# Kernel tuning notes

Hardware: AMD Instinct MI355X
Metric: run time of the kernel (lower is better)

The kernel has to match this reference:

```python
import jax, jax.numpy as jnp
import numpy as np

N = 50000      # nodes
E = 800000     # edges
G = 64         # graphs in batch
H = 256        # hidden_channels
CE = 128       # coord embed dim = H//2
OTH = 6        # in_channels - 3
ED = 8         # edge_dim
EE = 128       # edge_embedding_dim
GD = 16        # global_dim
L = 3          # num_layers


def setup_inputs() -> dict:
    key = jax.random.key(0)
    ks = jax.random.split(key, 24)
    s = 0.05
    inp = {
        "x": jax.random.normal(ks[0], (N, 9), jnp.float32),
        "edge_index": jax.random.randint(ks[1], (2, E), 0, N),
        "batch": jnp.sort(jax.random.randint(ks[2], (N,), 0, G)),
        "edge_attr": jax.random.normal(ks[3], (E, ED), jnp.float32),
        "global_x": jax.random.normal(ks[4], (G, GD), jnp.float32),
        # coordinate embedder (Linear 3->128 + relu)
        "coord_W": jax.random.normal(ks[5], (3, CE), jnp.float32) * s,
        "coord_b": jnp.zeros((CE,), jnp.float32),
        # node_mlp (Linear 6->128 + relu)
        "node_W": jax.random.normal(ks[6], (OTH, CE), jnp.float32) * s,
        "node_b": jnp.zeros((CE,), jnp.float32),
        # edge processor (Linear 8->128 + relu) and projection 128->256
        "edge_W": jax.random.normal(ks[7], (ED, EE), jnp.float32) * s,
        "edge_b": jnp.zeros((EE,), jnp.float32),
        "proj_W": jax.random.normal(ks[8], (EE, H), jnp.float32) * s,
        "proj_b": jnp.zeros((H,), jnp.float32),
        # stacked GCN layer weights
        "gcn_W": jax.random.normal(ks[9], (L, H, H), jnp.float32) * s,
        "gcn_b": jnp.zeros((L, H), jnp.float32),
        # attention pooling
        "attn_w": jax.random.normal(ks[10], (H,), jnp.float32) * s,
        "attn_b": jnp.zeros((), jnp.float32),
        # global_mlp: Linear 16->256, relu, Linear 256->256
        "gmlp_W1": jax.random.normal(ks[11], (GD, H), jnp.float32) * s,
        "gmlp_b1": jnp.zeros((H,), jnp.float32),
        "gmlp_W2": jax.random.normal(ks[12], (H, H), jnp.float32) * s,
        "gmlp_b2": jnp.zeros((H,), jnp.float32),
        # fc_out: Linear 512->256, relu, Linear 256->1
        "fc_W1": jax.random.normal(ks[13], (2 * H, H), jnp.float32) * s,
        "fc_b1": jnp.zeros((H,), jnp.float32),
        "fc_W2": jax.random.normal(ks[14], (H, 1), jnp.float32) * s,
        "fc_b2": jnp.zeros((1,), jnp.float32),
    }
    return inp


def _segsum(v, idx, num):
    return jax.ops.segment_sum(v, idx, num_segments=num)


def reference(x, edge_index, batch, edge_attr, global_x,
              coord_W, coord_b, node_W, node_b, edge_W, edge_b,
              proj_W, proj_b, gcn_W, gcn_b, attn_w, attn_b,
              gmlp_W1, gmlp_b1, gmlp_W2, gmlp_b2,
              fc_W1, fc_b1, fc_W2, fc_b2):
    relu = jax.nn.relu
    # --- node embedding: coords + other features ---
    coord_emb = relu(x[:, :3] @ coord_W + coord_b)          # [N, 128]
    other_emb = relu(x[:, 3:] @ node_W + node_b)            # [N, 128]
    x_emb = jnp.concatenate([coord_emb, other_emb], axis=1)  # [N, 256]

    # --- edge embedding, aggregated to target nodes (index_add over col) ---
    edge_emb = relu(edge_attr @ edge_W + edge_b) @ proj_W + proj_b  # [E, 256]
    col0 = edge_index[1]
    node_msg = _segsum(edge_emb, col0, N)                    # [N, 256]

    # --- GCN normalization with self-loops ---
    sl = jnp.arange(N)
    row = jnp.concatenate([edge_index[0], sl])
    col = jnp.concatenate([edge_index[1], sl])
    deg = _segsum(jnp.ones_like(col, jnp.float32), col, N)   # >= 1
    dnorm = jax.lax.rsqrt(deg)
    efac = (dnorm[row] * dnorm[col])[:, None]                # [E+N, 1]

    # --- stacked GCN layers (edge messages re-added each layer, per source) ---
    for i in range(L):
        x_in = x_emb + node_msg
        h = x_in @ gcn_W[i]                                  # [N, 256]
        x_emb = _segsum(h[row] * efac, col, N) + gcn_b[i]
        if i < L - 1:
            x_emb = relu(x_emb)

    # --- attention pooling (per-graph softmax over batch index) ---
    scores = x_emb @ attn_w + attn_b                         # [N]
    m = jax.ops.segment_max(scores, batch, num_segments=G)
    e = jnp.exp(scores - m[batch])
    denom = _segsum(e, batch, G)
    attn = e / denom[batch]
    graph_emb = _segsum(x_emb * attn[:, None], batch, G)     # [G, 256]

    # --- global features + head ---
    g = relu(global_x @ gmlp_W1 + gmlp_b1) @ gmlp_W2 + gmlp_b2
    hcat = jnp.concatenate([graph_emb, g], axis=-1)          # [G, 512]
    out = relu(hcat @ fc_W1 + fc_b1) @ fc_W2 + fc_b2         # [G, 1]
    return out
```

## Files before the change

### kernel.cpp

```cpp
#include <hip/hip_runtime.h>


typedef float f32x4 __attribute__((ext_vector_type(4)));
typedef short s16x8 __attribute__((ext_vector_type(8)));

__device__ __forceinline__ unsigned short f2bf(float f) {
  union { float f; unsigned u; } v{f};
  unsigned r = v.u + 0x7fff + ((v.u >> 16) & 1);
  return (unsigned short)(r >> 16);
}
__device__ __forceinline__ float bf2f(unsigned short s) {
  union { unsigned u; float f; } v{(unsigned)s << 16};
  return v.f;
}
__device__ __forceinline__ float blo(unsigned u) {
  union { unsigned x; float f; } v{u << 16};
  return v.f;
}
__device__ __forceinline__ float bhi(unsigned u) {
  union { unsigned x; float f; } v{u & 0xffff0000u};
  return v.f;
}
__device__ __forceinline__ unsigned pk2(float a, float b) {
  return (unsigned)f2bf(a) | ((unsigned)f2bf(b) << 16);
}

__global__ void node_embed_kernel(const float* __restrict__ x,
                                  const float* __restrict__ coord_W, const float* __restrict__ coord_b,
                                  const float* __restrict__ node_W, const float* __restrict__ node_b,
                                  short* __restrict__ x0, int N) {
  int tid = threadIdx.x;
  int node = blockIdx.x * 8 + (tid >> 5);
  if (node >= N) return;
  int ch0 = (tid & 31) * 8;
  const float* xr = x + (size_t)node * 9;
  float a[8];
  if (ch0 < 128) {
    float4 b0 = *(const float4*)&coord_b[ch0];
    float4 b1 = *(const float4*)&coord_b[ch0 + 4];
    a[0]=b0.x; a[1]=b0.y; a[2]=b0.z; a[3]=b0.w; a[4]=b1.x; a[5]=b1.y; a[6]=b1.z; a[7]=b1.w;
#pragma unroll
    for (int k = 0; k < 3; k++) {
      float xv = xr[k];
      float4 w0 = *(const float4*)&coord_W[k * 128 + ch0];
      float4 w1 = *(const float4*)&coord_W[k * 128 + ch0 + 4];
      a[0] = fmaf(xv, w0.x, a[0]); a[1] = fmaf(xv, w0.y, a[1]);
      a[2] = fmaf(xv, w0.z, a[2]); a[3] = fmaf(xv, w0.w, a[3]);
      a[4] = fmaf(xv, w1.x, a[4]); a[5] = fmaf(xv, w1.y, a[5]);
      a[6] = fmaf(xv, w1.z, a[6]); a[7] = fmaf(xv, w1.w, a[7]);
    }
  } else {
    int c0 = ch0 - 128;
    float4 b0 = *(const float4*)&node_b[c0];
    float4 b1 = *(const float4*)&node_b[c0 + 4];
    a[0]=b0.x; a[1]=b0.y; a[2]=b0.z; a[3]=b0.w; a[4]=b1.x; a[5]=b1.y; a[6]=b1.z; a[7]=b1.w;
#pragma unroll
    for (int k = 0; k < 6; k++) {
      float xv = xr[3 + k];
      float4 w0 = *(const float4*)&node_W[k * 128 + c0];
      float4 w1 = *(const float4*)&node_W[k * 128 + c0 + 4];
      a[0] = fmaf(xv, w0.x, a[0]); a[1] = fmaf(xv, w0.y, a[1]);
      a[2] = fmaf(xv, w0.z, a[2]); a[3] = fmaf(xv, w0.w, a[3]);
      a[4] = fmaf(xv, w1.x, a[4]); a[5] = fmaf(xv, w1.y, a[5]);
      a[6] = fmaf(xv, w1.z, a[6]); a[7] = fmaf(xv, w1.w, a[7]);
    }
  }
  uint4 o;
  o.x = pk2(fmaxf(a[0], 0.f), fmaxf(a[1], 0.f));
  o.y = pk2(fmaxf(a[2], 0.f), fmaxf(a[3], 0.f));
  o.z = pk2(fmaxf(a[4], 0.f), fmaxf(a[5], 0.f));
  o.w = pk2(fmaxf(a[6], 0.f), fmaxf(a[7], 0.f));
  *(uint4*)&x0[(size_t)node * 256 + ch0] = o;
}

__global__ void count_kernel(const int* __restrict__ col, int* __restrict__ cnt, int E) {
  int e = blockIdx.x * 256 + threadIdx.x;
  if (e < E) atomicAdd(&cnt[col[e]], 1);
}

__global__ void breduce_kernel(const int* __restrict__ cnt, int* __restrict__ partials, int N) {
  __shared__ int red[256];
  int t = threadIdx.x;
  int i = blockIdx.x * 256 + t;
  int v = (i < N) ? cnt[i] : 0;
  red[t] = v;
  __syncthreads();
  for (int off = 128; off; off >>= 1) {
    if (t < off) red[t] += red[t + off];
    __syncthreads();
  }
  if (t == 0) partials[blockIdx.x] = red[0];
}

__global__ void scan_partials_kernel(int* __restrict__ partials, int nb) {
  __shared__ int s[1024];
  int t = threadIdx.x;
  for (int i = t; i < nb; i += 256) s[i] = partials[i];
  __syncthreads();
  if (t == 0) {
    int run = 0;
    for (int i = 0; i < nb; i++) { int c = s[i]; s[i] = run; run += c; }
  }
  __syncthreads();
  for (int i = t; i < nb; i += 256) partials[i] = s[i];
}

__global__ void scan_apply_kernel(const int* __restrict__ cnt, const int* __restrict__ partials,
                                  int* __restrict__ rowstart, float* __restrict__ dnorm,
                                  int* __restrict__ cursor, int N) {
  __shared__ int red[256];
  int t = threadIdx.x;
  int i = blockIdx.x * 256 + t;
  int v = (i < N) ? cnt[i] : 0;
  red[t] = v;
  __syncthreads();
  for (int off = 1; off < 256; off <<= 1) {
    int x = (t >= off) ? red[t - off] : 0;
    __syncthreads();
    red[t] += x;
    __syncthreads();
  }
  if (i < N) {
    int ex = red[t] - v + partials[blockIdx.x];
    rowstart[i] = ex;
    dnorm[i] = rsqrtf((float)(v + 1));
    cursor[i] = 0;
    if (i == N - 1) rowstart[N] = ex + v;
  }
}

__global__ void scatter_kernel(const int* __restrict__ row, const int* __restrict__ col,
                               const int* __restrict__ rowstart, int* __restrict__ cursor,
                               const float* __restrict__ dnorm,
                               int2* __restrict__ pk8, int* __restrict__ eids, int E) {
  int e = blockIdx.x * 256 + threadIdx.x;
  if (e >= E) return;
  int c = col[e], r = row[e];
  int p = atomicAdd(&cursor[c], 1);
  int slot = rowstart[c] + p;
  pk8[slot] = make_int2(r, __float_as_int(dnorm[r] * dnorm[c]));
  eids[slot] = e;
}

__global__ void wt_kernel(const float* __restrict__ gcn_W, const float* __restrict__ proj_W,
                          short* __restrict__ gcnWt, short* __restrict__ projWt) {
  int idx = blockIdx.x * 256 + threadIdx.x;
  if (idx < 3 * 65536) {
    int l = idx >> 16, r = idx & 65535, n = r >> 8, k = r & 255;
    gcnWt[idx] = (short)f2bf(gcn_W[l * 65536 + k * 256 + n]);
  } else {
    int j = idx - 3 * 65536;
    int n = j >> 7, k = j & 127;
    projWt[j] = (short)f2bf(proj_W[k * 256 + n]);
  }
}

__global__ void __launch_bounds__(256) edge_msg_kernel(
    const float* __restrict__ edge_attr, const int* __restrict__ eids,
    const int* __restrict__ rowstart,
    const float* __restrict__ edge_W, const float* __restrict__ edge_b,
    unsigned* __restrict__ msg128u, int N) {
  int lane = threadIdx.x & 63;
  int node = blockIdx.x * 4 + (threadIdx.x >> 6);
  if (node >= N) return;
  int ch0 = lane * 2;
  float wa[8], wb[8];
#pragma unroll
  for (int k = 0; k < 8; k++) {
    float2 w = *(const float2*)&edge_W[k * 128 + ch0];
    wa[k] = w.x; wb[k] = w.y;
  }
  float2 bb = *(const float2*)&edge_b[ch0];
  float acc0 = 0.f, acc1 = 0.f;
  int s = rowstart[node], s1 = rowstart[node + 1];
  const float4* ea4 = (const float4*)edge_attr;
  for (; s + 4 <= s1; s += 4) {
    int e0 = eids[s], e1 = eids[s + 1], e2 = eids[s + 2], e3 = eids[s + 3];
    float4 a00 = ea4[(size_t)e0 * 2], a01 = ea4[(size_t)e0 * 2 + 1];
    float4 a10 = ea4[(size_t)e1 * 2], a11 = ea4[(size_t)e1 * 2 + 1];
    float4 a20 = ea4[(size_t)e2 * 2], a21 = ea4[(size_t)e2 * 2 + 1];
    float4 a30 = ea4[(size_t)e3 * 2], a31 = ea4[(size_t)e3 * 2 + 1];
    float t0, t1;
#define EMLP(lo, hi)                                                        \
    t0 = bb.x; t1 = bb.y;                                                   \
    t0 = fmaf(lo.x, wa[0], t0); t1 = fmaf(lo.x, wb[0], t1);                 \
    t0 = fmaf(lo.y, wa[1], t0); t1 = fmaf(lo.y, wb[1], t1);                 \
    t0 = fmaf(lo.z, wa[2], t0); t1 = fmaf(lo.z, wb[2], t1);                 \
    t0 = fmaf(lo.w, wa[3], t0); t1 = fmaf(lo.w, wb[3], t1);                 \
    t0 = fmaf(hi.x, wa[4], t0); t1 = fmaf(hi.x, wb[4], t1);                 \
    t0 = fmaf(hi.y, wa[5], t0); t1 = fmaf(hi.y, wb[5], t1);                 \
    t0 = fmaf(hi.z, wa[6], t0); t1 = fmaf(hi.z, wb[6], t1);                 \
    t0 = fmaf(hi.w, wa[7], t0); t1 = fmaf(hi.w, wb[7], t1);                 \
    acc0 += fmaxf(t0, 0.f); acc1 += fmaxf(t1, 0.f);
    EMLP(a00, a01)
    EMLP(a10, a11)
    EMLP(a20, a21)
    EMLP(a30, a31)
  }
  for (; s < s1; s++) {
    int e = eids[s];
    float4 lo = ea4[(size_t)e * 2], hi = ea4[(size_t)e * 2 + 1];
    float t0, t1;
    EMLP(lo, hi)
  }
#undef EMLP
  msg128u[(size_t)node * 64 + lane] = pk2(acc0, acc1);
}

__global__ void __launch_bounds__(256) proj_gemm_mfma(
    const short* __restrict__ msg128, const short* __restrict__ projWt,
    const float* __restrict__ proj_b, const int* __restrict__ cnt,
    short* __restrict__ node_msg, int N) {
  __shared__ short As[64][136];
  __shared__ short Bs[64][136];
  int tid = threadIdx.x;
  int n0 = blockIdx.x * 64;
  int cb = blockIdx.y * 64;
  for (int i = tid; i < 64 * 32; i += 256) {
    int r = i >> 5, c4 = (i & 31) << 2;
    int n = n0 + r;
    uint2 v = make_uint2(0, 0);
    if (n < N) v = *(const uint2*)&msg128[(size_t)n * 128 + c4];
    *(uint2*)&As[r][c4] = v;
    *(uint2*)&Bs[r][c4] = *(const uint2*)&projWt[(size_t)(cb + r) * 128 + c4];
  }
  __syncthreads();
  int wave = tid >> 6, lane = tid & 63;
  int mrow = wave * 16 + (lane & 15);
  int brow = lane & 15;
  int kgrp = (lane >> 4) * 8;
  f32x4 acc[4];
#pragma unroll
  for (int i = 0; i < 4; i++) acc[i] = (f32x4){0.f, 0.f, 0.f, 0.f};
#pragma unroll
  for (int kk = 0; kk < 4; kk++) {
    s16x8 a = *(const s16x8*)&As[mrow][kk * 32 + kgrp];
#pragma unroll
    for (int nf = 0; nf < 4; nf++) {
      s16x8 b = *(const s16x8*)&Bs[nf * 16 + brow][kk * 32 + kgrp];
      acc[nf] = __builtin_amdgcn_mfma_f32_16x16x32_bf16(a, b, acc[nf], 0, 0, 0);
    }
  }
  int orow0 = wave * 16 + (lane >> 4) * 4;
  int ocol = lane & 15;
#pragma unroll
  for (int r = 0; r < 4; r++) {
    int n = n0 + orow0 + r;
    if (n < N) {
      float cn = (float)cnt[n];
#pragma unroll
      for (int nf = 0; nf < 4; nf++) {
        int c = cb + nf * 16 + ocol;
        node_msg[(size_t)n * 256 + c] = (short)f2bf(acc[nf][r] + cn * proj_b[c]);
      }
    }
  }
}

__global__ void __launch_bounds__(256) gcn_gemm_add_mfma(
    const short* __restrict__ X, const short* __restrict__ M,
    const short* __restrict__ Wt, short* __restrict__ Hout, int N) {
  __shared__ short As[64][264];
  __shared__ short Bs[64][264];
  int tid = threadIdx.x;
  int n0 = blockIdx.x * 64;
  int cb = blockIdx.y * 64;
  for (int i = tid; i < 64 * 64; i += 256) {
    int r = i >> 6, c4 = (i & 63) << 2;
    int n = n0 + r;
    uint2 o = make_uint2(0, 0);
    if (n < N) {
      uint2 xv = *(const uint2*)&X[(size_t)n * 256 + c4];
      uint2 mv = *(const uint2*)&M[(size_t)n * 256 + c4];
      o.x = pk2(blo(xv.x) + blo(mv.x), bhi(xv.x) + bhi(mv.x));
      o.y = pk2(blo(xv.y) + blo(mv.y), bhi(xv.y) + bhi(mv.y));
    }
    *(uint2*)&As[r][c4] = o;
    *(uint2*)&Bs[r][c4] = *(const uint2*)&Wt[(size_t)(cb + r) * 256 + c4];
  }
  __syncthreads();
  int wave = tid >> 6, lane = tid & 63;
  int mrow = wave * 16 + (lane & 15);
  int brow = lane & 15;
  int kgrp = (lane >> 4) * 8;
  f32x4 acc[4];
#pragma unroll
  for (int i = 0; i < 4; i++) acc[i] = (f32x4){0.f, 0.f, 0.f, 0.f};
#pragma unroll
  for (int kk = 0; kk < 8; kk++) {
    s16x8 a = *(const s16x8*)&As[mrow][kk * 32 + kgrp];
#pragma unroll
    for (int nf = 0; nf < 4; nf++) {
      s16x8 b = *(const s16x8*)&Bs[nf * 16 + brow][kk * 32 + kgrp];
      acc[nf] = __builtin_amdgcn_mfma_f32_16x16x32_bf16(a, b, acc[nf], 0, 0, 0);
    }
  }
  int orow0 = wave * 16 + (lane >> 4) * 4;
  int ocol = lane & 15;
#pragma unroll
  for (int nf = 0; nf < 4; nf++) {
#pragma unroll
    for (int r = 0; r < 4; r++) {
      int n = n0 + orow0 + r;
      if (n < N) Hout[(size_t)n * 256 + cb + nf * 16 + ocol] = (short)f2bf(acc[nf][r]);
    }
  }
}

__global__ void __launch_bounds__(256) gcn_gemm_mfma(
    const short* __restrict__ Xin, const short* __restrict__ Wt,
    short* __restrict__ Hout, int N) {
  __shared__ short As[64][264];
  __shared__ short Bs[64][264];
  int tid = threadIdx.x;
  int n0 = blockIdx.x * 64;
  int cb = blockIdx.y * 64;
  for (int i = tid; i < 64 * 64; i += 256) {
    int r = i >> 6, c4 = (i & 63) << 2;
    int n = n0 + r;
    uint2 v = make_uint2(0, 0);
    if (n < N) v = *(const uint2*)&Xin[(size_t)n * 256 + c4];
    *(uint2*)&As[r][c4] = v;
    *(uint2*)&Bs[r][c4] = *(const uint2*)&Wt[(size_t)(cb + r) * 256 + c4];
  }
  __syncthreads();
  int wave = tid >> 6, lane = tid & 63;
  int mrow = wave * 16 + (lane & 15);
  int brow = lane & 15;
  int kgrp = (lane >> 4) * 8;
  f32x4 acc[4];
#pragma unroll
  for (int i = 0; i < 4; i++) acc[i] = (f32x4){0.f, 0.f, 0.f, 0.f};
#pragma unroll
  for (int kk = 0; kk < 8; kk++) {
    s16x8 a = *(const s16x8*)&As[mrow][kk * 32 + kgrp];
#pragma unroll
    for (int nf = 0; nf < 4; nf++) {
      s16x8 b = *(const s16x8*)&Bs[nf * 16 + brow][kk * 32 + kgrp];
      acc[nf] = __builtin_amdgcn_mfma_f32_16x16x32_bf16(a, b, acc[nf], 0, 0, 0);
    }
  }
  int orow0 = wave * 16 + (lane >> 4) * 4;
  int ocol = lane & 15;
#pragma unroll
  for (int nf = 0; nf < 4; nf++) {
#pragma unroll
    for (int r = 0; r < 4; r++) {
      int n = n0 + orow0 + r;
      if (n < N) Hout[(size_t)n * 256 + cb + nf * 16 + ocol] = (short)f2bf(acc[nf][r]);
    }
  }
}

__global__ void __launch_bounds__(256) gcn_agg_kernel(
    const short* __restrict__ h, const int2* __restrict__ pk8,
    const int* __restrict__ rowstart, const float* __restrict__ dnorm,
    const float* __restrict__ b, const short* __restrict__ node_msg,
    short* __restrict__ xin, int N) {
  int lane = threadIdx.x & 63;
  int node = blockIdx.x * 4 + (threadIdx.x >> 6);
  if (node >= N) return;
  int ch0 = lane << 2;
  size_t rowb = (size_t)node * 256 + ch0;
  float dn = dnorm[node];
  float wgt = dn * dn;
  uint2 hv = *(const uint2*)&h[rowb];
  float a0 = blo(hv.x) * wgt, a1 = bhi(hv.x) * wgt;
  float a2 = blo(hv.y) * wgt, a3 = bhi(hv.y) * wgt;
  int s = rowstart[node], s1 = rowstart[node + 1];
  for (; s + 4 <= s1; s += 4) {
    int2 p0 = pk8[s], p1 = pk8[s + 1], p2 = pk8[s + 2], p3 = pk8[s + 3];
    float f0 = __int_as_float(p0.y), f1 = __int_as_float(p1.y);
    float f2 = __int_as_float(p2.y), f3 = __int_as_float(p3.y);
    uint2 v0 = *(const uint2*)&h[(size_t)p0.x * 256 + ch0];
    uint2 v1 = *(const uint2*)&h[(size_t)p1.x * 256 + ch0];
    uint2 v2 = *(const uint2*)&h[(size_t)p2.x * 256 + ch0];
    uint2 v3 = *(const uint2*)&h[(size_t)p3.x * 256 + ch0];
    a0 = fmaf(blo(v0.x), f0, a0); a1 = fmaf(bhi(v0.x), f0, a1);
    a2 = fmaf(blo(v0.y), f0, a2); a3 = fmaf(bhi(v0.y), f0, a3);
    a0 = fmaf(blo(v1.x), f1, a0); a1 = fmaf(bhi(v1.x), f1, a1);
    a2 = fmaf(blo(v1.y), f1, a2); a3 = fmaf(bhi(v1.y), f1, a3);
    a0 = fmaf(blo(v2.x), f2, a0); a1 = fmaf(bhi(v2.x), f2, a1);
    a2 = fmaf(blo(v2.y), f2, a2); a3 = fmaf(bhi(v2.y), f2, a3);
    a0 = fmaf(blo(v3.x), f3, a0); a1 = fmaf(bhi(v3.x), f3, a1);
    a2 = fmaf(blo(v3.y), f3, a2); a3 = fmaf(bhi(v3.y), f3, a3);
  }
  for (; s < s1; s++) {
    int2 p = pk8[s];
    float f = __int_as_float(p.y);
    uint2 v = *(const uint2*)&h[(size_t)p.x * 256 + ch0];
    a0 = fmaf(blo(v.x), f, a0); a1 = fmaf(bhi(v.x), f, a1);
    a2 = fmaf(blo(v.y), f, a2); a3 = fmaf(bhi(v.y), f, a3);
  }
  float4 bv = *(const float4*)&b[ch0];
  uint2 mv = *(const uint2*)&node_msg[rowb];
  float y0 = fmaxf(a0 + bv.x, 0.f) + blo(mv.x);
  float y1 = fmaxf(a1 + bv.y, 0.f) + bhi(mv.x);
  float y2 = fmaxf(a2 + bv.z, 0.f) + blo(mv.y);
  float y3 = fmaxf(a3 + bv.w, 0.f) + bhi(mv.y);
  uint2 o;
  o.x = pk2(y0, y1);
  o.y = pk2(y2, y3);
  *(uint2*)&xin[rowb] = o;
}

__global__ void __launch_bounds__(256) final_agg_kernel(
    const short* __restrict__ h, const int2* __restrict__ pk8,
    const int* __restrict__ rowstart, const float* __restrict__ dnorm,
    const float* __restrict__ b, short* __restrict__ x_emb,
    const float* __restrict__ attn_w, const float* __restrict__ attn_b,
    float* __restrict__ scores, int N) {
  int lane = threadIdx.x & 63;
  int node = blockIdx.x * 4 + (threadIdx.x >> 6);
  if (node >= N) return;
  int ch0 = lane << 2;
  size_t rowb = (size_t)node * 256 + ch0;
  float dn = dnorm[node];
  float wgt = dn * dn;
  uint2 hv = *(const uint2*)&h[rowb];
  float a0 = blo(hv.x) * wgt, a1 = bhi(hv.x) * wgt;
  float a2 = blo(hv.y) * wgt, a3 = bhi(hv.y) * wgt;
  int s = rowstart[node], s1 = rowstart[node + 1];
  for (; s + 4 <= s1; s += 4) {
    int2 p0 = pk8[s], p1 = pk8[s + 1], p2 = pk8[s + 2], p3 = pk8[s + 3];
    float f0 = __int_as_float(p0.y), f1 = __int_as_float(p1.y);
    float f2 = __int_as_float(p2.y), f3 = __int_as_float(p3.y);
    uint2 v0 = *(const uint2*)&h[(size_t)p0.x * 256 + ch0];
    uint2 v1 = *(const uint2*)&h[(size_t)p1.x * 256 + ch0];
    uint2 v2 = *(const uint2*)&h[(size_t)p2.x * 256 + ch0];
    uint2 v3 = *(const uint2*)&h[(size_t)p3.x * 256 + ch0];
    a0 = fmaf(blo(v0.x), f0, a0); a1 = fmaf(bhi(v0.x), f0, a1);
    a2 = fmaf(blo(v0.y), f0, a2); a3 = fmaf(bhi(v0.y), f0, a3);
    a0 = fmaf(blo(v1.x), f1, a0); a1 = fmaf(bhi(v1.x), f1, a1);
    a2 = fmaf(blo(v1.y), f1, a2); a3 = fmaf(bhi(v1.y), f1, a3);
    a0 = fmaf(blo(v2.x), f2, a0); a1 = fmaf(bhi(v2.x), f2, a1);
    a2 = fmaf(blo(v2.y), f2, a2); a3 = fmaf(bhi(v2.y), f2, a3);
    a0 = fmaf(blo(v3.x), f3, a0); a1 = fmaf(bhi(v3.x), f3, a1);
    a2 = fmaf(blo(v3.y), f3, a2); a3 = fmaf(bhi(v3.y), f3, a3);
  }
  for (; s < s1; s++) {
    int2 p = pk8[s];
    float f = __int_as_float(p.y);
    uint2 v = *(const uint2*)&h[(size_t)p.x * 256 + ch0];
    a0 = fmaf(blo(v.x), f, a0); a1 = fmaf(bhi(v.x), f, a1);
    a2 = fmaf(blo(v.y), f, a2); a3 = fmaf(bhi(v.y), f, a3);
  }
  float4 bv = *(const float4*)&b[ch0];
  a0 += bv.x; a1 += bv.y; a2 += bv.z; a3 += bv.w;
  uint2 o;
  o.x = pk2(a0, a1);
  o.y = pk2(a2, a3);
  *(uint2*)&x_emb[rowb] = o;
  float4 aw = *(const float4*)&attn_w[ch0];
  float p = a0 * aw.x + a1 * aw.y + a2 * aw.z + a3 * aw.w;
#pragma unroll
  for (int off = 32; off; off >>= 1) p += __shfl_down(p, off);
  if (lane == 0) scores[node] = p + attn_b[0];
}

__global__ void gse_kernel(const int* __restrict__ batch, int* __restrict__ gs,
                           int* __restrict__ ge, int N) {
  int i = blockIdx.x * 256 + threadIdx.x;
  if (i >= N) return;
  int g = batch[i];
  if (i == 0) gs[g] = 0;
  else {
    int gp = batch[i - 1];
    if (gp != g) { gs[g] = i; ge[gp] = i - 1; }
  }
  if (i == N - 1) ge[g] = N - 1;
}

__global__ void softmax_kernel(const float* __restrict__ scores, const int* __restrict__ gs,
                               const int* __restrict__ ge, float* __restrict__ wnode) {
  int g = blockIdx.x;
  int tid = threadIdx.x;
  __shared__ float red[256];
  int s0 = gs[g], e1 = ge[g];
  if (s0 > e1) return;
  int s1 = e1 + 1;
  float m = -1e30f;
  for (int i = s0 + tid; i < s1; i += 256) m = fmaxf(m, scores[i]);
  red[tid] = m;
  __syncthreads();
  for (int off = 128; off; off >>= 1) {
    if (tid < off) red[tid] = fmaxf(red[tid], red[tid + off]);
    __syncthreads();
  }
  m = red[0];
  __syncthreads();
  float d = 0.f;
  for (int i = s0 + tid; i < s1; i += 256) d += expf(scores[i] - m);
  red[tid] = d;
  __syncthreads();
  for (int off = 128; off; off >>= 1) {
    if (tid < off) red[tid] += red[tid + off];
    __syncthreads();
  }
  float rd = 1.f / red[0];
  for (int i = s0 + tid; i < s1; i += 256) wnode[i] = expf(scores[i] - m) * rd;
}

__global__ void __launch_bounds__(256) pool_sum_kernel(
    const short* __restrict__ x_emb, const float* __restrict__ wnode,
    const int* __restrict__ batch, float* __restrict__ graph_emb, int N) {
  __shared__ int sb[256];
  __shared__ float sw[256];
  int ch = threadIdx.x;
  int i0 = blockIdx.x * 256;
  int lim = min(256, N - i0);
  if (ch < lim) { sb[ch] = batch[i0 + ch]; sw[ch] = wnode[i0 + ch]; }
  __syncthreads();
  int curg = sb[0];
  float acc = 0.f;
  for (int j = 0; j < lim; j++) {
    int g = sb[j];
    if (g != curg) {
      atomicAdd(&graph_emb[(size_t)curg * 256 + ch], acc);
      acc = 0.f;
      curg = g;
    }
    acc = fmaf(bf2f((unsigned short)x_emb[(size_t)(i0 + j) * 256 + ch]), sw[j], acc);
  }
  atomicAdd(&graph_emb[(size_t)curg * 256 + ch], acc);
}

__global__ void head_kernel(const float* __restrict__ global_x, const float* __restrict__ graph_emb,
                            const float* __restrict__ W1, const float* __restrict__ b1,
                            const float* __restrict__ W2, const float* __restrict__ b2,
                            const float* __restrict__ fW1, const float* __restrict__ fb1,
                            const float* __restrict__ fW2, const float* __restrict__ fb2,
                            float* __restrict__ out) {
  int g = blockIdx.x;
  int ch = threadIdx.x;
  __shared__ float t1[256], g2s[256], t3s[256];
  float a = b1[ch];
  const float* gx = global_x + g * 16;
#pragma unroll
  for (int k = 0; k < 16; k++) a = fmaf(gx[k], W1[k * 256 + ch], a);
  t1[ch] = fmaxf(a, 0.f);
  __syncthreads();
  float bb = b2[ch];
  for (int k = 0; k < 256; k++) bb = fmaf(t1[k], W2[k * 256 + ch], bb);
  g2s[ch] = bb;
  __syncthreads();
  float c = fb1[ch];
  const float* ger = graph_emb + (size_t)g * 256;
  for (int k = 0; k < 256; k++) c = fmaf(ger[k], fW1[k * 256 + ch], c);
  for (int k = 0; k < 256; k++) c = fmaf(g2s[k], fW1[(256 + k) * 256 + ch], c);
  t3s[ch] = fmaxf(c, 0.f);
  __syncthreads();
  t1[ch] = t3s[ch] * fW2[ch];
  __syncthreads();
  for (int off = 128; off; off >>= 1) {
    if (ch < off) t1[ch] += t1[ch + off];
    __syncthreads();
  }
  if (ch == 0) out[g] = t1[0] + fb2[0];
}

extern "C" void kernel_launch(void* const* d_in, const int* in_sizes, int n_in,
                              void* d_out, int out_size, void* d_ws, size_t ws_size,
                              hipStream_t stream) {
  const float* x        = (const float*)d_in[0];
  const int*   ei       = (const int*)d_in[1];
  const int*   batch    = (const int*)d_in[2];
  const float* edge_attr= (const float*)d_in[3];
  const float* global_x = (const float*)d_in[4];
  const float* coord_W  = (const float*)d_in[5];
  const float* coord_b  = (const float*)d_in[6];
  const float* node_W   = (const float*)d_in[7];
  const float* node_b   = (const float*)d_in[8];
  const float* edge_W   = (const float*)d_in[9];
  const float* edge_b   = (const float*)d_in[10];
  const float* proj_W   = (const float*)d_in[11];
  const float* proj_b   = (const float*)d_in[12];
  const float* gcn_W    = (const float*)d_in[13];
  const float* gcn_b    = (const float*)d_in[14];
  const float* attn_w   = (const float*)d_in[15];
  const float* attn_b   = (const float*)d_in[16];
  const float* gmlp_W1  = (const float*)d_in[17];
  const float* gmlp_b1  = (const float*)d_in[18];
  const float* gmlp_W2  = (const float*)d_in[19];
  const float* gmlp_b2  = (const float*)d_in[20];
  const float* fc_W1    = (const float*)d_in[21];
  const float* fc_b1    = (const float*)d_in[22];
  const float* fc_W2    = (const float*)d_in[23];
  const float* fc_b2    = (const float*)d_in[24];

  const int N = in_sizes[0] / 9;
  const int E = in_sizes[3] / 8;
  const int G = in_sizes[4] / 16;
  const int NB = (N + 255) / 256;
  const int NM = (N + 63) / 64;

  char* w = (char*)d_ws;
  auto alloc = [&](size_t bytes) -> char* {
    char* p = w;
    w += (bytes + 255) & ~(size_t)255;
    return p;
  };
  short* x0       = (short*)alloc((size_t)N * 256 * 2);
  short* node_msg = (short*)alloc((size_t)N * 256 * 2);
  short* hA       = (short*)alloc((size_t)N * 256 * 2);
  short* hB       = (short*)alloc((size_t)N * 256 * 2);
  short* xinBuf   = (short*)alloc((size_t)N * 256 * 2);
  short* x_emb    = (short*)alloc((size_t)N * 256 * 2);
  short* msg128   = x_emb;
  int2*  pk8      = (int2*)alloc((size_t)E * 8);
  int*   eids     = (int*)alloc((size_t)E * 4);
  short* gcnWt    = (short*)alloc((size_t)3 * 65536 * 2);
  short* projWt   = (short*)alloc((size_t)256 * 128 * 2);
  int*   cnt      = (int*)alloc((size_t)N * 4);
  int*   rowstart = (int*)alloc((size_t)(N + 1) * 4);
  int*   cursor   = (int*)alloc((size_t)N * 4);
  float* dnorm    = (float*)alloc((size_t)N * 4);
  float* scores   = (float*)alloc((size_t)N * 4);
  float* wnode    = (float*)alloc((size_t)N * 4);
  int*   partials = (int*)alloc((size_t)NB * 4);
  int*   gs       = (int*)alloc((size_t)G * 4);
  int*   ge       = (int*)alloc((size_t)G * 4);
  float* graph_emb= (float*)alloc((size_t)G * 256 * 4);

  hipMemsetAsync(cnt, 0, (size_t)N * 4, stream);
  hipMemsetAsync(gs, 0x7f, (size_t)G * 4, stream);
  hipMemsetAsync(ge, 0xff, (size_t)G * 4, stream);
  hipMemsetAsync(graph_emb, 0, (size_t)G * 256 * 4, stream);

  wt_kernel<<<(3 * 65536 + 256 * 128 + 255) / 256, 256, 0, stream>>>(gcn_W, proj_W, gcnWt, projWt);
  node_embed_kernel<<<(N + 7) / 8, 256, 0, stream>>>(
      x, coord_W, coord_b, node_W, node_b, x0, N);
  count_kernel<<<(E + 255) / 256, 256, 0, stream>>>(ei + E, cnt, E);
  breduce_kernel<<<NB, 256, 0, stream>>>(cnt, partials, N);
  scan_partials_kernel<<<1, 256, 0, stream>>>(partials, NB);
  scan_apply_kernel<<<NB, 256, 0, stream>>>(cnt, partials, rowstart, dnorm, cursor, N);
  scatter_kernel<<<(E + 255) / 256, 256, 0, stream>>>(
      ei, ei + E, rowstart, cursor, dnorm, pk8, eids, E);
  edge_msg_kernel<<<(N + 3) / 4, 256, 0, stream>>>(
      edge_attr, eids, rowstart, edge_W, edge_b, (unsigned*)msg128, N);
  proj_gemm_mfma<<<dim3(NM, 4), 256, 0, stream>>>(
      msg128, projWt, proj_b, cnt, node_msg, N);
  gcn_gemm_add_mfma<<<dim3(NM, 4), 256, 0, stream>>>(
      x0, node_msg, gcnWt, hA, N);
  gcn_agg_kernel<<<(N + 3) / 4, 256, 0, stream>>>(
      hA, pk8, rowstart, dnorm, gcn_b, node_msg, xinBuf, N);
  gcn_gemm_mfma<<<dim3(NM, 4), 256, 0, stream>>>(
      xinBuf, gcnWt + 65536, hB, N);
  gcn_agg_kernel<<<(N + 3) / 4, 256, 0, stream>>>(
      hB, pk8, rowstart, dnorm, gcn_b + 256, node_msg, xinBuf, N);
  gcn_gemm_mfma<<<dim3(NM, 4), 256, 0, stream>>>(
      xinBuf, gcnWt + 2 * 65536, hA, N);
  final_agg_kernel<<<(N + 3) / 4, 256, 0, stream>>>(
      hA, pk8, rowstart, dnorm, gcn_b + 512, x_emb, attn_w, attn_b, scores, N);
  gse_kernel<<<(N + 255) / 256, 256, 0, stream>>>(batch, gs, ge, N);
  softmax_kernel<<<G, 256, 0, stream>>>(scores, gs, ge, wnode);
  pool_sum_kernel<<<NB, 256, 0, stream>>>(x_emb, wnode, batch, graph_emb, N);
  head_kernel<<<G, 256, 0, stream>>>(global_x, graph_emb, gmlp_W1, gmlp_b1, gmlp_W2, gmlp_b2,
                                     fc_W1, fc_b1, fc_W2, fc_b2, (float*)d_out);
}
```

Measured before the change: 867.1 us.

## Compute all output column blocks per row tile, keeping A fragments in registers

The three MFMA GEMM kernels (proj, gcn with add, gcn) now launch one block per 64-row tile instead of a 2D grid with four column blocks. Each block loads its A tile once, keeps the A fragments in registers, and loops over the four 64-column weight slices, reloading B into shared memory each time. This removes the fourfold redundant global reads of the activation rows and the repeated add of X+M, in exchange for four times fewer blocks, extra barriers, and serialized B loads inside each block.

```diff
diff --git a/kernel.cpp b/kernel.cpp
--- a/kernel.cpp
+++ b/kernel.cpp
@@ -215,43 +215,56 @@
   __shared__ short Bs[64][136];
   int tid = threadIdx.x;
   int n0 = blockIdx.x * 64;
-  int cb = blockIdx.y * 64;
   for (int i = tid; i < 64 * 32; i += 256) {
     int r = i >> 5, c4 = (i & 31) << 2;
     int n = n0 + r;
     uint2 v = make_uint2(0, 0);
     if (n < N) v = *(const uint2*)&msg128[(size_t)n * 128 + c4];
     *(uint2*)&As[r][c4] = v;
-    *(uint2*)&Bs[r][c4] = *(const uint2*)&projWt[(size_t)(cb + r) * 128 + c4];
   }
   __syncthreads();
   int wave = tid >> 6, lane = tid & 63;
   int mrow = wave * 16 + (lane & 15);
   int brow = lane & 15;
   int kgrp = (lane >> 4) * 8;
-  f32x4 acc[4];
-#pragma unroll
-  for (int i = 0; i < 4; i++) acc[i] = (f32x4){0.f, 0.f, 0.f, 0.f};
-#pragma unroll
-  for (int kk = 0; kk < 4; kk++) {
-    s16x8 a = *(const s16x8*)&As[mrow][kk * 32 + kgrp];
-#pragma unroll
-    for (int nf = 0; nf < 4; nf++) {
-      s16x8 b = *(const s16x8*)&Bs[nf * 16 + brow][kk * 32 + kgrp];
-      acc[nf] = __builtin_amdgcn_mfma_f32_16x16x32_bf16(a, b, acc[nf], 0, 0, 0);
-    }
-  }
+  s16x8 areg[4];
+#pragma unroll
+  for (int kk = 0; kk < 4; kk++) areg[kk] = *(const s16x8*)&As[mrow][kk * 32 + kgrp];
   int orow0 = wave * 16 + (lane >> 4) * 4;
   int ocol = lane & 15;
+  float cn[4];
 #pragma unroll
   for (int r = 0; r < 4; r++) {
     int n = n0 + orow0 + r;
-    if (n < N) {
-      float cn = (float)cnt[n];
+    cn[r] = (n < N) ? (float)cnt[n] : 0.f;
+  }
+  for (int cb = 0; cb < 4; cb++) {
+    __syncthreads();
+    for (int i = tid; i < 64 * 32; i += 256) {
+      int r = i >> 5, c4 = (i & 31) << 2;
+      *(uint2*)&Bs[r][c4] = *(const uint2*)&projWt[(size_t)(cb * 64 + r) * 128 + c4];
+    }
+    __syncthreads();
+    f32x4 acc[4];
+#pragma unroll
+    for (int i = 0; i < 4; i++) acc[i] = (f32x4){0.f, 0.f, 0.f, 0.f};
+#pragma unroll
+    for (int kk = 0; kk < 4; kk++) {
 #pragma unroll
       for (int nf = 0; nf < 4; nf++) {
-        int c = cb + nf * 16 + ocol;
-        node_msg[(size_t)n * 256 + c] = (short)f2bf(acc[nf][r] + cn * proj_b[c]);
+        s16x8 b = *(const s16x8*)&Bs[nf * 16 + brow][kk * 32 + kgrp];
+        acc[nf] = __builtin_amdgcn_mfma_f32_16x16x32_bf16(areg[kk], b, acc[nf], 0, 0, 0);
+      }
+    }
+#pragma unroll
+    for (int r = 0; r < 4; r++) {
+      int n = n0 + orow0 + r;
+      if (n < N) {
+#pragma unroll
+        for (int nf = 0; nf < 4; nf++) {
+          int c = cb * 64 + nf * 16 + ocol;
+          node_msg[(size_t)n * 256 + c] = (short)f2bf(acc[nf][r] + cn[r] * proj_b[c]);
+        }
       }
     }
   }
@@ -264,7 +277,6 @@
   __shared__ short Bs[64][264];
   int tid = threadIdx.x;
   int n0 = blockIdx.x * 64;
-  int cb = blockIdx.y * 64;
   for (int i = tid; i < 64 * 64; i += 256) {
     int r = i >> 6, c4 = (i & 63) << 2;
     int n = n0 + r;
@@ -276,33 +288,42 @@
       o.y = pk2(blo(xv.y) + blo(mv.y), bhi(xv.y) + bhi(mv.y));
     }
     *(uint2*)&As[r][c4] = o;
-    *(uint2*)&Bs[r][c4] = *(const uint2*)&Wt[(size_t)(cb + r) * 256 + c4];
   }
   __syncthreads();
   int wave = tid >> 6, lane = tid & 63;
   int mrow = wave * 16 + (lane & 15);
   int brow = lane & 15;
   int kgrp = (lane >> 4) * 8;
-  f32x4 acc[4];
-#pragma unroll
-  for (int i = 0; i < 4; i++) acc[i] = (f32x4){0.f, 0.f, 0.f, 0.f};
-#pragma unroll
-  for (int kk = 0; kk < 8; kk++) {
-    s16x8 a = *(const s16x8*)&As[mrow][kk * 32 + kgrp];
-#pragma unroll
-    for (int nf = 0; nf < 4; nf++) {
-      s16x8 b = *(const s16x8*)&Bs[nf * 16 + brow][kk * 32 + kgrp];
-      acc[nf] = __builtin_amdgcn_mfma_f32_16x16x32_bf16(a, b, acc[nf], 0, 0, 0);
-    }
-  }
+  s16x8 areg[8];
+#pragma unroll
+  for (int kk = 0; kk < 8; kk++) areg[kk] = *(const s16x8*)&As[mrow][kk * 32 + kgrp];
   int orow0 = wave * 16 + (lane >> 4) * 4;
   int ocol = lane & 15;
-#pragma unroll
-  for (int nf = 0; nf < 4; nf++) {
-#pragma unroll
-    for (int r = 0; r < 4; r++) {
-      int n = n0 + orow0 + r;
-      if (n < N) Hout[(size_t)n * 256 + cb + nf * 16 + ocol] = (short)f2bf(acc[nf][r]);
+  for (int cb = 0; cb < 4; cb++) {
+    __syncthreads();
+    for (int i = tid; i < 64 * 64; i += 256) {
+      int r = i >> 6, c4 = (i & 63) << 2;
+      *(uint2*)&Bs[r][c4] = *(const uint2*)&Wt[(size_t)(cb * 64 + r) * 256 + c4];
+    }
+    __syncthreads();
+    f32x4 acc[4];
+#pragma unroll
+    for (int i = 0; i < 4; i++) acc[i] = (f32x4){0.f, 0.f, 0.f, 0.f};
+#pragma unroll
+    for (int kk = 0; kk < 8; kk++) {
+#pragma unroll
+      for (int nf = 0; nf < 4; nf++) {
+        s16x8 b = *(const s16x8*)&Bs[nf * 16 + brow][kk * 32 + kgrp];
+        acc[nf] = __builtin_amdgcn_mfma_f32_16x16x32_bf16(areg[kk], b, acc[nf], 0, 0, 0);
+      }
+    }
+#pragma unroll
+    for (int nf = 0; nf < 4; nf++) {
+#pragma unroll
+      for (int r = 0; r < 4; r++) {
+        int n = n0 + orow0 + r;
+        if (n < N) Hout[(size_t)n * 256 + cb * 64 + nf * 16 + ocol] = (short)f2bf(acc[nf][r]);
+      }
     }
   }
 }
@@ -314,40 +335,48 @@
   __shared__ short Bs[64][264];
   int tid = threadIdx.x;
   int n0 = blockIdx.x * 64;
-  int cb = blockIdx.y * 64;
   for (int i = tid; i < 64 * 64; i += 256) {
     int r = i >> 6, c4 = (i & 63) << 2;
     int n = n0 + r;
     uint2 v = make_uint2(0, 0);
     if (n < N) v = *(const uint2*)&Xin[(size_t)n * 256 + c4];
     *(uint2*)&As[r][c4] = v;
-    *(uint2*)&Bs[r][c4] = *(const uint2*)&Wt[(size_t)(cb + r) * 256 + c4];
   }
   __syncthreads();
   int wave = tid >> 6, lane = tid & 63;
   int mrow = wave * 16 + (lane & 15);
   int brow = lane & 15;
   int kgrp = (lane >> 4) * 8;
-  f32x4 acc[4];
-#pragma unroll
-  for (int i = 0; i < 4; i++) acc[i] = (f32x4){0.f, 0.f, 0.f, 0.f};
-#pragma unroll
-  for (int kk = 0; kk < 8; kk++) {
-    s16x8 a = *(const s16x8*)&As[mrow][kk * 32 + kgrp];
-#pragma unroll
-    for (int nf = 0; nf < 4; nf++) {
-      s16x8 b = *(const s16x8*)&Bs[nf * 16 + brow][kk * 32 + kgrp];
-      acc[nf] = __builtin_amdgcn_mfma_f32_16x16x32_bf16(a, b, acc[nf], 0, 0, 0);
-    }
-  }
+  s16x8 areg[8];
+#pragma unroll
+  for (int kk = 0; kk < 8; kk++) areg[kk] = *(const s16x8*)&As[mrow][kk * 32 + kgrp];
   int orow0 = wave * 16 + (lane >> 4) * 4;
   int ocol = lane & 15;
-#pragma unroll
-  for (int nf = 0; nf < 4; nf++) {
-#pragma unroll
-    for (int r = 0; r < 4; r++) {
-      int n = n0 + orow0 + r;
-      if (n < N) Hout[(size_t)n * 256 + cb + nf * 16 + ocol] = (short)f2bf(acc[nf][r]);
+  for (int cb = 0; cb < 4; cb++) {
+    __syncthreads();
+    for (int i = tid; i < 64 * 64; i += 256) {
+      int r = i >> 6, c4 = (i & 63) << 2;
+      *(uint2*)&Bs[r][c4] = *(const uint2*)&Wt[(size_t)(cb * 64 + r) * 256 + c4];
+    }
+    __syncthreads();
+    f32x4 acc[4];
+#pragma unroll
+    for (int i = 0; i < 4; i++) acc[i] = (f32x4){0.f, 0.f, 0.f, 0.f};
+#pragma unroll
+    for (int kk = 0; kk < 8; kk++) {
+#pragma unroll
+      for (int nf = 0; nf < 4; nf++) {
+        s16x8 b = *(const s16x8*)&Bs[nf * 16 + brow][kk * 32 + kgrp];
+        acc[nf] = __builtin_amdgcn_mfma_f32_16x16x32_bf16(areg[kk], b, acc[nf], 0, 0, 0);
+      }
+    }
+#pragma unroll
+    for (int nf = 0; nf < 4; nf++) {
+#pragma unroll
+      for (int r = 0; r < 4; r++) {
+        int n = n0 + orow0 + r;
+        if (n < N) Hout[(size_t)n * 256 + cb * 64 + nf * 16 + ocol] = (short)f2bf(acc[nf][r]);
+      }
     }
   }
 }
@@ -638,17 +667,17 @@
       ei, ei + E, rowstart, cursor, dnorm, pk8, eids, E);
   edge_msg_kernel<<<(N + 3) / 4, 256, 0, stream>>>(
       edge_attr, eids, rowstart, edge_W, edge_b, (unsigned*)msg128, N);
-  proj_gemm_mfma<<<dim3(NM, 4), 256, 0, stream>>>(
+  proj_gemm_mfma<<<NM, 256, 0, stream>>>(
       msg128, projWt, proj_b, cnt, node_msg, N);
-  gcn_gemm_add_mfma<<<dim3(NM, 4), 256, 0, stream>>>(
+  gcn_gemm_add_mfma<<<NM, 256, 0, stream>>>(
       x0, node_msg, gcnWt, hA, N);
   gcn_agg_kernel<<<(N + 3) / 4, 256, 0, stream>>>(
       hA, pk8, rowstart, dnorm, gcn_b, node_msg, xinBuf, N);
-  gcn_gemm_mfma<<<dim3(NM, 4), 256, 0, stream>>>(
+  gcn_gemm_mfma<<<NM, 256, 0, stream>>>(
       xinBuf, gcnWt + 65536, hB, N);
   gcn_agg_kernel<<<(N + 3) / 4, 256, 0, stream>>>(
       hB, pk8, rowstart, dnorm, gcn_b + 256, node_msg, xinBuf, N);
-  gcn_gemm_mfma<<<dim3(NM, 4), 256, 0, stream>>>(
+  gcn_gemm_mfma<<<NM, 256, 0, stream>>>(
       xinBuf, gcnWt + 2 * 65536, hA, N);
   final_agg_kernel<<<(N + 3) / 4, 256, 0, stream>>>(
       hA, pk8, rowstart, dnorm, gcn_b + 512, x_emb, attn_w, attn_b, scores, N);
```

After: 819.6 us. 5.5% less time.
